# Optimization experiments

Hardware: AMD Instinct MI355X
Metric: run time of the kernel (lower is better)

Reference implementation:

```python
import jax, jax.numpy as jnp
import numpy as np

DECAY = 0.99
EPSILON = 1e-05
CODEBOOK_SIZE = 1024


def setup_inputs() -> dict:
    key = jax.random.key(0)
    k1, k2, k3 = jax.random.split(key, 3)
    B, T, D, K = 8, 4096, 128, CODEBOOK_SIZE
    return {
        "x": jax.random.normal(k1, (B, T, D), dtype=jnp.float32),
        "embed": jax.random.normal(k2, (K, D), dtype=jnp.float32),
        "cluster_size": jnp.ones((K,), dtype=jnp.float32),
        "embed_avg": jax.random.normal(k3, (K, D), dtype=jnp.float32),
    }


def reference(x, embed, cluster_size, embed_avg):
    shape = x.shape
    K, D = embed.shape
    flat = x.reshape(-1, D)  # (N, D)

    dist = 2.0 * (flat @ embed.T) - jnp.sum(flat * flat, axis=1, keepdims=True) \
           - jnp.sum(embed * embed, axis=1)[None, :]  # (N, K)
    embed_ind_flat = jnp.argmax(dist, axis=-1)  # (N,) int
    embed_ind = embed_ind_flat.reshape(shape[:-1])
    quantize = embed[embed_ind]  # dequantize via gather, (B, T, D)

    # training EMA updates (one-hot scatter expressed as segment sums)
    counts = jax.ops.segment_sum(jnp.ones_like(embed_ind_flat, dtype=x.dtype),
                                 embed_ind_flat, num_segments=K)  # == onehot.sum(0)
    embed_sum = jax.ops.segment_sum(flat, embed_ind_flat, num_segments=K)  # == (x.T @ onehot).T

    new_cluster_size = cluster_size * DECAY + (1.0 - DECAY) * counts
    new_embed_avg = embed_avg * DECAY + (1.0 - DECAY) * embed_sum

    total = new_cluster_size.sum()
    smoothed = (new_cluster_size + EPSILON) / (total + K * EPSILON) * total
    new_embed = new_embed_avg / smoothed[:, None]

    return quantize, embed_ind, new_cluster_size, new_embed_avg, new_embed
```

## Files before the change

### kernel.cpp

```cpp
#include <hip/hip_runtime.h>

#define NROWS 32768
#define DDIM  128
#define KCODES 1024
#define DECAY 0.99f
#define OMD   0.01f
#define EPS   1e-5f

typedef __attribute__((ext_vector_type(8))) short short8;
typedef __attribute__((ext_vector_type(4))) float f32x4;

#define WS_COUNTS 0
#define WS_OFFS   1024
#define WS_CURSOR 2048
#define WS_INV    3072
#define WS_EN2H   4096
#define WS_BUCKET 5120

__device__ __forceinline__ unsigned short f2bf(float f) {
  union { float f; unsigned int u; } cv; cv.f = f;
  unsigned int u = cv.u;
  return (unsigned short)((u + 0x7fffu + ((u >> 16) & 1u)) >> 16);
}

__global__ __launch_bounds__(256) void pack_e(const float* __restrict__ embed,
                                              ushort* __restrict__ epack,
                                              float* __restrict__ en2h) {
  const int tid = threadIdx.x;
  const int w = tid >> 6, lane = tid & 63;
  const int nt = blockIdx.x * 4 + w;
  const int m = lane & 15, q = lane >> 4;
  const int row = nt * 16 + m;
  const float* ep = embed + (size_t)row * DDIM + q * 8;
  float ss = 0.f;
  #pragma unroll
  for (int kb = 0; kb < 4; ++kb) {
    float4 v0 = *(const float4*)(ep + kb * 32);
    float4 v1 = *(const float4*)(ep + kb * 32 + 4);
    float v[8] = {v0.x, v0.y, v0.z, v0.w, v1.x, v1.y, v1.z, v1.w};
    unsigned int h[8], l[8];
    #pragma unroll
    for (int j = 0; j < 8; ++j) {
      ss += v[j] * v[j];
      h[j] = f2bf(v[j]);
      float fh = __uint_as_float(h[j] << 16);
      l[j] = f2bf(v[j] - fh);
    }
    uint4 ph, pl;
    ph.x = h[0] | (h[1] << 16); ph.y = h[2] | (h[3] << 16);
    ph.z = h[4] | (h[5] << 16); ph.w = h[6] | (h[7] << 16);
    pl.x = l[0] | (l[1] << 16); pl.y = l[2] | (l[3] << 16);
    pl.z = l[4] | (l[5] << 16); pl.w = l[6] | (l[7] << 16);
    *(uint4*)(epack + (((size_t)nt * 8 + kb) * 64 + lane) * 8)     = ph;
    *(uint4*)(epack + (((size_t)nt * 8 + kb + 4) * 64 + lane) * 8) = pl;
  }
  ss += __shfl_xor(ss, 16, 64);
  ss += __shfl_xor(ss, 32, 64);
  if (q == 0) en2h[row] = 0.5f * ss;
}

__global__ __launch_bounds__(256)
__attribute__((amdgpu_waves_per_eu(2, 2)))
void vq_mfma(
    const float* __restrict__ x, const short8* __restrict__ ep8,
    const float* __restrict__ en2h,
    float* __restrict__ counts, float* __restrict__ out_ind) {
  __shared__ unsigned long long keys[4][64];
  const int tid = threadIdx.x;
  const int w = tid >> 6, lane = tid & 63;
  const int c = lane & 15, q = lane >> 4;
  const int mt0 = blockIdx.x * 4;
  const int nt0 = w * 16;

  short8 a[4][8];
  #pragma unroll
  for (int t = 0; t < 4; ++t) {
    const float* xp = x + (size_t)((mt0 + t) * 16 + c) * DDIM + q * 8;
    #pragma unroll
    for (int kb = 0; kb < 4; ++kb) {
      float4 v0 = *(const float4*)(xp + kb * 32);
      float4 v1 = *(const float4*)(xp + kb * 32 + 4);
      float v[8] = {v0.x, v0.y, v0.z, v0.w, v1.x, v1.y, v1.z, v1.w};
      short8 hh, ll;
      #pragma unroll
      for (int j = 0; j < 8; ++j) {
        unsigned int hv = f2bf(v[j]);
        hh[j] = (short)hv;
        float fh = __uint_as_float(hv << 16);
        ll[j] = (short)f2bf(v[j] - fh);
      }
      a[t][kb] = hh;
      a[t][kb + 4] = ll;
    }
  }

  float bestv[16]; int besti[16];
  #pragma unroll
  for (int i = 0; i < 16; ++i) { bestv[i] = -3.4e38f; besti[i] = 0; }

  for (int ch = 0; ch < 16; ++ch) {
    const int nt = nt0 + ch;
    short8 st[8];
    #pragma unroll
    for (int j = 0; j < 8; ++j)
      st[j] = ep8[((size_t)nt * 8 + j) * 64 + lane];
    const float nh = en2h[nt * 16 + c];
    f32x4 acc[4];
    #pragma unroll
    for (int t = 0; t < 4; ++t) acc[t] = (f32x4){0.f, 0.f, 0.f, 0.f};
    #pragma unroll
    for (int t = 0; t < 4; ++t) {
      #pragma unroll
      for (int kb = 0; kb < 4; ++kb)
        acc[t] = __builtin_amdgcn_mfma_f32_16x16x32_bf16(a[t][kb], st[kb], acc[t], 0, 0, 0);
      #pragma unroll
      for (int kb = 0; kb < 4; ++kb)
        acc[t] = __builtin_amdgcn_mfma_f32_16x16x32_bf16(a[t][4 + kb], st[kb], acc[t], 0, 0, 0);
      #pragma unroll
      for (int kb = 0; kb < 4; ++kb)
        acc[t] = __builtin_amdgcn_mfma_f32_16x16x32_bf16(a[t][kb], st[4 + kb], acc[t], 0, 0, 0);
    }
    const int code = nt * 16 + c;
    #pragma unroll
    for (int t = 0; t < 4; ++t)
      #pragma unroll
      for (int r = 0; r < 4; ++r) {
        float s = acc[t][r] - nh;
        int i = t * 4 + r;
        if (s > bestv[i]) { bestv[i] = s; besti[i] = code; }
      }
  }

  #pragma unroll
  for (int off = 1; off < 16; off <<= 1) {
    #pragma unroll
    for (int i = 0; i < 16; ++i) {
      float ov = __shfl_xor(bestv[i], off, 64);
      int   oi = __shfl_xor(besti[i], off, 64);
      if (ov > bestv[i] || (ov == bestv[i] && oi < besti[i])) {
        bestv[i] = ov; besti[i] = oi;
      }
    }
  }
  if (c == 0) {
    #pragma unroll
    for (int t = 0; t < 4; ++t)
      #pragma unroll
      for (int r = 0; r < 4; ++r) {
        unsigned u = __float_as_uint(bestv[t * 4 + r]);
        unsigned su = (u & 0x80000000u) ? ~u : (u | 0x80000000u);
        keys[w][t * 16 + q * 4 + r] =
            ((unsigned long long)su << 32) |
            (unsigned long long)(0xFFFFFFFFu - (unsigned)besti[t * 4 + r]);
      }
  }
  __syncthreads();
  if (tid < 64) {
    unsigned long long k0 = keys[0][tid], k1 = keys[1][tid];
    unsigned long long k2 = keys[2][tid], k3 = keys[3][tid];
    unsigned long long k = k0 > k1 ? k0 : k1;
    if (k2 > k) k = k2;
    if (k3 > k) k = k3;
    int code = (int)(0xFFFFFFFFu - (unsigned)(k & 0xFFFFFFFFull));
    out_ind[blockIdx.x * 64 + tid] = (float)code;
    unsafeAtomicAdd(counts + code, 1.0f);
  }
}

__global__ void scan_fin(const float* __restrict__ counts, const float* __restrict__ cs,
                         int* __restrict__ offs, int* __restrict__ cursor,
                         float* __restrict__ out_ncs, float* __restrict__ inv) {
  __shared__ float wtot[16];
  __shared__ float ctot[16];
  int tid = threadIdx.x;
  int lane = tid & 63, w = tid >> 6;
  float cnum = counts[tid];
  float cv = cs[tid];
  float s = cnum;
  #pragma unroll
  for (int off = 1; off < 64; off <<= 1) {
    float v = __shfl_up(s, off, 64);
    if (lane >= off) s += v;
  }
  float r2 = cv;
  #pragma unroll
  for (int off = 32; off > 0; off >>= 1) r2 += __shfl_down(r2, off, 64);
  if (lane == 63) wtot[w] = s;
  if (lane == 0)  ctot[w] = r2;
  __syncthreads();
  if (tid < 16) {
    float v = wtot[tid];
    #pragma unroll
    for (int off = 1; off < 16; off <<= 1) {
      float p = __shfl_up(v, off, 64);
      if (tid >= off) v += p;
    }
    wtot[tid] = v;
    float t2 = ctot[tid];
    #pragma unroll
    for (int off = 8; off > 0; off >>= 1) t2 += __shfl_down(t2, off, 64);
    if (tid == 0) ctot[0] = t2;
  }
  __syncthreads();
  float prefix = (w > 0) ? wtot[w - 1] : 0.f;
  int excl = (int)(s + prefix) - (int)cnum;
  offs[tid] = excl;
  cursor[tid] = excl;
  float ncs = cv * DECAY + OMD * cnum;
  out_ncs[tid] = ncs;
  float total = ctot[0] * DECAY + OMD * (float)NROWS;
  inv[tid] = (total + (float)KCODES * EPS) / ((ncs + EPS) * total);
}

__global__ void scatter_rows(const float* __restrict__ out_ind,
                             int* __restrict__ cursor, int* __restrict__ bucket) {
  int row = blockIdx.x * 256 + threadIdx.x;
  int code = (int)out_ind[row];
  int pos = atomicAdd(cursor + code, 1);
  bucket[pos] = row;
}

__global__ __launch_bounds__(256) void esum_q_fin(
    const int* __restrict__ bucket, const int* __restrict__ offs,
    const float* __restrict__ counts, const float* __restrict__ x,
    const float* __restrict__ embed, const float* __restrict__ ea,
    const float* __restrict__ inv,
    float* __restrict__ out_q, float* __restrict__ out_nea, float* __restrict__ out_ne) {
  __shared__ float4 part[512];
  const int code = blockIdx.x;
  const int t = threadIdx.x;
  const int c8 = t & 15;
  const int h = t >> 4;
  const int start = offs[code];
  const int cnt = (int)counts[code];
  const float4 e0 = *(const float4*)(embed + (size_t)code * DDIM + c8 * 8);
  const float4 e1 = *(const float4*)(embed + (size_t)code * DDIM + c8 * 8 + 4);
  float4 a0 = {0.f, 0.f, 0.f, 0.f}, a1 = {0.f, 0.f, 0.f, 0.f};
  int i = h;
  for (; i + 16 < cnt; i += 32) {
    int rowA = bucket[start + i];
    int rowB = bucket[start + i + 16];
    const float* pa = x + (size_t)rowA * DDIM + c8 * 8;
    const float* pb = x + (size_t)rowB * DDIM + c8 * 8;
    float4 xa0 = *(const float4*)(pa), xa1 = *(const float4*)(pa + 4);
    float4 xb0 = *(const float4*)(pb), xb1 = *(const float4*)(pb + 4);
    float* qa = out_q + (size_t)rowA * DDIM + c8 * 8;
    float* qb = out_q + (size_t)rowB * DDIM + c8 * 8;
    *(float4*)(qa) = e0; *(float4*)(qa + 4) = e1;
    *(float4*)(qb) = e0; *(float4*)(qb + 4) = e1;
    a0.x += xa0.x + xb0.x; a0.y += xa0.y + xb0.y; a0.z += xa0.z + xb0.z; a0.w += xa0.w + xb0.w;
    a1.x += xa1.x + xb1.x; a1.y += xa1.y + xb1.y; a1.z += xa1.z + xb1.z; a1.w += xa1.w + xb1.w;
  }
  for (; i < cnt; i += 16) {
    int row = bucket[start + i];
    const float* pa = x + (size_t)row * DDIM + c8 * 8;
    float4 xa0 = *(const float4*)(pa), xa1 = *(const float4*)(pa + 4);
    float* qa = out_q + (size_t)row * DDIM + c8 * 8;
    *(float4*)(qa) = e0; *(float4*)(qa + 4) = e1;
    a0.x += xa0.x; a0.y += xa0.y; a0.z += xa0.z; a0.w += xa0.w;
    a1.x += xa1.x; a1.y += xa1.y; a1.z += xa1.z; a1.w += xa1.w;
  }
  part[h * 32 + c8 * 2]     = a0;
  part[h * 32 + c8 * 2 + 1] = a1;
  __syncthreads();
  if (t < 32) {
    float4 s = part[t];
    #pragma unroll
    for (int hh = 1; hh < 16; ++hh) {
      float4 p = part[hh * 32 + t];
      s.x += p.x; s.y += p.y; s.z += p.z; s.w += p.w;
    }
    float iv = inv[code];
    int base = code * DDIM + t * 4;
    float4 a = *(const float4*)(ea + base);
    float4 nea;
    nea.x = a.x * DECAY + OMD * s.x; nea.y = a.y * DECAY + OMD * s.y;
    nea.z = a.z * DECAY + OMD * s.z; nea.w = a.w * DECAY + OMD * s.w;
    *(float4*)(out_nea + base) = nea;
    float4 ne;
    ne.x = nea.x * iv; ne.y = nea.y * iv; ne.z = nea.z * iv; ne.w = nea.w * iv;
    *(float4*)(out_ne + base) = ne;
  }
}

extern "C" void kernel_launch(void* const* d_in, const int* in_sizes, int n_in,
                              void* d_out, int out_size, void* d_ws, size_t ws_size,
                              hipStream_t stream) {
  const float* x     = (const float*)d_in[0];
  const float* embed = (const float*)d_in[1];
  const float* cs    = (const float*)d_in[2];
  const float* ea    = (const float*)d_in[3];

  float* out     = (float*)d_out;
  float* out_q   = out;
  float* out_ind = out_q + 4194304;
  float* out_ncs = out_ind + 32768;
  float* out_nea = out_ncs + 1024;
  float* out_ne  = out_nea + 131072;

  float* ws     = (float*)d_ws;
  float* counts = ws + WS_COUNTS;
  int*   offs   = (int*)(ws + WS_OFFS);
  int*   cursor = (int*)(ws + WS_CURSOR);
  float* inv    = ws + WS_INV;
  float* en2h   = ws + WS_EN2H;
  int*   bucket = (int*)(ws + WS_BUCKET);

  ushort* epack = (ushort*)out_nea;

  hipMemsetAsync(counts, 0, KCODES * sizeof(float), stream);
  pack_e<<<16, 256, 0, stream>>>(embed, epack, en2h);
  vq_mfma<<<NROWS / 64, 256, 0, stream>>>(x, (const short8*)epack, en2h, counts, out_ind);
  scan_fin<<<1, 1024, 0, stream>>>(counts, cs, offs, cursor, out_ncs, inv);
  scatter_rows<<<NROWS / 256, 256, 0, stream>>>(out_ind, cursor, bucket);
  esum_q_fin<<<KCODES, 256, 0, stream>>>(bucket, offs, counts, x, embed, ea, inv,
                                         out_q, out_nea, out_ne);
}
```

Baseline: 184.8 us.

## Fuse codebook packing into VQ kernel and merge histogram, scan and scatter

Removes the separate pack_e kernel: each wave now loads fp32 codebook rows directly, computes their half-norms and splits them into bf16 hi/lo inside the distance loop. M-tile per block drops from 64 to 32 rows, which doubles the grid and reduces accumulator registers. The global-atomic count, scan and scatter kernels become one single-block kernel that builds the histogram and bucket list with shared-memory atomics. This removes a memset and three launches, but the codebook is now re-converted by every block, and the bucket scatter runs serially in a single workgroup.

```diff
diff --git a/kernel.cpp b/kernel.cpp
--- a/kernel.cpp
+++ b/kernel.cpp
@@ -12,69 +12,27 @@
 
 #define WS_COUNTS 0
 #define WS_OFFS   1024
-#define WS_CURSOR 2048
-#define WS_INV    3072
-#define WS_EN2H   4096
-#define WS_BUCKET 5120
-
-__device__ __forceinline__ unsigned short f2bf(float f) {
+#define WS_INV    2048
+#define WS_BUCKET 3072
+
+__device__ __forceinline__ unsigned int f2bf(float f) {
   union { float f; unsigned int u; } cv; cv.f = f;
   unsigned int u = cv.u;
-  return (unsigned short)((u + 0x7fffu + ((u >> 16) & 1u)) >> 16);
-}
-
-__global__ __launch_bounds__(256) void pack_e(const float* __restrict__ embed,
-                                              ushort* __restrict__ epack,
-                                              float* __restrict__ en2h) {
-  const int tid = threadIdx.x;
-  const int w = tid >> 6, lane = tid & 63;
-  const int nt = blockIdx.x * 4 + w;
-  const int m = lane & 15, q = lane >> 4;
-  const int row = nt * 16 + m;
-  const float* ep = embed + (size_t)row * DDIM + q * 8;
-  float ss = 0.f;
-  #pragma unroll
-  for (int kb = 0; kb < 4; ++kb) {
-    float4 v0 = *(const float4*)(ep + kb * 32);
-    float4 v1 = *(const float4*)(ep + kb * 32 + 4);
-    float v[8] = {v0.x, v0.y, v0.z, v0.w, v1.x, v1.y, v1.z, v1.w};
-    unsigned int h[8], l[8];
-    #pragma unroll
-    for (int j = 0; j < 8; ++j) {
-      ss += v[j] * v[j];
-      h[j] = f2bf(v[j]);
-      float fh = __uint_as_float(h[j] << 16);
-      l[j] = f2bf(v[j] - fh);
-    }
-    uint4 ph, pl;
-    ph.x = h[0] | (h[1] << 16); ph.y = h[2] | (h[3] << 16);
-    ph.z = h[4] | (h[5] << 16); ph.w = h[6] | (h[7] << 16);
-    pl.x = l[0] | (l[1] << 16); pl.y = l[2] | (l[3] << 16);
-    pl.z = l[4] | (l[5] << 16); pl.w = l[6] | (l[7] << 16);
-    *(uint4*)(epack + (((size_t)nt * 8 + kb) * 64 + lane) * 8)     = ph;
-    *(uint4*)(epack + (((size_t)nt * 8 + kb + 4) * 64 + lane) * 8) = pl;
-  }
-  ss += __shfl_xor(ss, 16, 64);
-  ss += __shfl_xor(ss, 32, 64);
-  if (q == 0) en2h[row] = 0.5f * ss;
-}
-
-__global__ __launch_bounds__(256)
-__attribute__((amdgpu_waves_per_eu(2, 2)))
-void vq_mfma(
-    const float* __restrict__ x, const short8* __restrict__ ep8,
-    const float* __restrict__ en2h,
-    float* __restrict__ counts, float* __restrict__ out_ind) {
-  __shared__ unsigned long long keys[4][64];
+  return (u + 0x7fffu + ((u >> 16) & 1u)) >> 16;
+}
+
+__global__ __launch_bounds__(256) void vq_mfma(
+    const float* __restrict__ x, const float* __restrict__ embed,
+    float* __restrict__ out_ind) {
+  __shared__ unsigned long long keys[4][32];
   const int tid = threadIdx.x;
   const int w = tid >> 6, lane = tid & 63;
   const int c = lane & 15, q = lane >> 4;
-  const int mt0 = blockIdx.x * 4;
-  const int nt0 = w * 16;
-
-  short8 a[4][8];
-  #pragma unroll
-  for (int t = 0; t < 4; ++t) {
+  const int mt0 = blockIdx.x * 2;
+
+  short8 a[2][8];
+  #pragma unroll
+  for (int t = 0; t < 2; ++t) {
     const float* xp = x + (size_t)((mt0 + t) * 16 + c) * DDIM + q * 8;
     #pragma unroll
     for (int kb = 0; kb < 4; ++kb) {
@@ -94,47 +52,66 @@
     }
   }
 
-  float bestv[16]; int besti[16];
-  #pragma unroll
-  for (int i = 0; i < 16; ++i) { bestv[i] = -3.4e38f; besti[i] = 0; }
-
+  float bestv[8]; int besti[8];
+  #pragma unroll
+  for (int i = 0; i < 8; ++i) { bestv[i] = -3.4e38f; besti[i] = 0; }
+
+  const int cbase = w * 256;
   for (int ch = 0; ch < 16; ++ch) {
-    const int nt = nt0 + ch;
-    short8 st[8];
-    #pragma unroll
-    for (int j = 0; j < 8; ++j)
-      st[j] = ep8[((size_t)nt * 8 + j) * 64 + lane];
-    const float nh = en2h[nt * 16 + c];
-    f32x4 acc[4];
-    #pragma unroll
-    for (int t = 0; t < 4; ++t) acc[t] = (f32x4){0.f, 0.f, 0.f, 0.f};
-    #pragma unroll
-    for (int t = 0; t < 4; ++t) {
+    const int crow = cbase + ch * 16 + c;
+    const float* ep = embed + (size_t)crow * DDIM + q * 8;
+    float nhq = 0.f;
+    short8 sh[4], sl[4];
+    #pragma unroll
+    for (int kb = 0; kb < 4; ++kb) {
+      float4 v0 = *(const float4*)(ep + kb * 32);
+      float4 v1 = *(const float4*)(ep + kb * 32 + 4);
+      float v[8] = {v0.x, v0.y, v0.z, v0.w, v1.x, v1.y, v1.z, v1.w};
+      short8 hh, ll;
       #pragma unroll
-      for (int kb = 0; kb < 4; ++kb)
-        acc[t] = __builtin_amdgcn_mfma_f32_16x16x32_bf16(a[t][kb], st[kb], acc[t], 0, 0, 0);
-      #pragma unroll
-      for (int kb = 0; kb < 4; ++kb)
-        acc[t] = __builtin_amdgcn_mfma_f32_16x16x32_bf16(a[t][4 + kb], st[kb], acc[t], 0, 0, 0);
-      #pragma unroll
-      for (int kb = 0; kb < 4; ++kb)
-        acc[t] = __builtin_amdgcn_mfma_f32_16x16x32_bf16(a[t][kb], st[4 + kb], acc[t], 0, 0, 0);
-    }
-    const int code = nt * 16 + c;
-    #pragma unroll
-    for (int t = 0; t < 4; ++t)
-      #pragma unroll
-      for (int r = 0; r < 4; ++r) {
-        float s = acc[t][r] - nh;
-        int i = t * 4 + r;
-        if (s > bestv[i]) { bestv[i] = s; besti[i] = code; }
-      }
+      for (int j = 0; j < 8; ++j) {
+        nhq += v[j] * v[j];
+        unsigned int hv = f2bf(v[j]);
+        hh[j] = (short)hv;
+        float fh = __uint_as_float(hv << 16);
+        ll[j] = (short)f2bf(v[j] - fh);
+      }
+      sh[kb] = hh;
+      sl[kb] = ll;
+    }
+    nhq += __shfl_xor(nhq, 16, 64);
+    nhq += __shfl_xor(nhq, 32, 64);
+    const float nh = 0.5f * nhq;
+
+    f32x4 acc0 = {0.f, 0.f, 0.f, 0.f}, acc1 = {0.f, 0.f, 0.f, 0.f};
+    #pragma unroll
+    for (int kb = 0; kb < 4; ++kb) {
+      acc0 = __builtin_amdgcn_mfma_f32_16x16x32_bf16(a[0][kb], sh[kb], acc0, 0, 0, 0);
+      acc1 = __builtin_amdgcn_mfma_f32_16x16x32_bf16(a[1][kb], sh[kb], acc1, 0, 0, 0);
+    }
+    #pragma unroll
+    for (int kb = 0; kb < 4; ++kb) {
+      acc0 = __builtin_amdgcn_mfma_f32_16x16x32_bf16(a[0][kb + 4], sh[kb], acc0, 0, 0, 0);
+      acc1 = __builtin_amdgcn_mfma_f32_16x16x32_bf16(a[1][kb + 4], sh[kb], acc1, 0, 0, 0);
+    }
+    #pragma unroll
+    for (int kb = 0; kb < 4; ++kb) {
+      acc0 = __builtin_amdgcn_mfma_f32_16x16x32_bf16(a[0][kb], sl[kb], acc0, 0, 0, 0);
+      acc1 = __builtin_amdgcn_mfma_f32_16x16x32_bf16(a[1][kb], sl[kb], acc1, 0, 0, 0);
+    }
+    #pragma unroll
+    for (int r = 0; r < 4; ++r) {
+      float s0 = acc0[r] - nh;
+      if (s0 > bestv[r])     { bestv[r] = s0;     besti[r] = crow; }
+      float s1 = acc1[r] - nh;
+      if (s1 > bestv[4 + r]) { bestv[4 + r] = s1; besti[4 + r] = crow; }
+    }
   }
 
   #pragma unroll
   for (int off = 1; off < 16; off <<= 1) {
     #pragma unroll
-    for (int i = 0; i < 16; ++i) {
+    for (int i = 0; i < 8; ++i) {
       float ov = __shfl_xor(bestv[i], off, 64);
       int   oi = __shfl_xor(besti[i], off, 64);
       if (ov > bestv[i] || (ov == bestv[i] && oi < besti[i])) {
@@ -144,7 +121,7 @@
   }
   if (c == 0) {
     #pragma unroll
-    for (int t = 0; t < 4; ++t)
+    for (int t = 0; t < 2; ++t)
       #pragma unroll
       for (int r = 0; r < 4; ++r) {
         unsigned u = __float_as_uint(bestv[t * 4 + r]);
@@ -155,27 +132,38 @@
       }
   }
   __syncthreads();
-  if (tid < 64) {
+  if (tid < 32) {
     unsigned long long k0 = keys[0][tid], k1 = keys[1][tid];
     unsigned long long k2 = keys[2][tid], k3 = keys[3][tid];
     unsigned long long k = k0 > k1 ? k0 : k1;
     if (k2 > k) k = k2;
     if (k3 > k) k = k3;
     int code = (int)(0xFFFFFFFFu - (unsigned)(k & 0xFFFFFFFFull));
-    out_ind[blockIdx.x * 64 + tid] = (float)code;
-    unsafeAtomicAdd(counts + code, 1.0f);
-  }
-}
-
-__global__ void scan_fin(const float* __restrict__ counts, const float* __restrict__ cs,
-                         int* __restrict__ offs, int* __restrict__ cursor,
-                         float* __restrict__ out_ncs, float* __restrict__ inv) {
-  __shared__ float wtot[16];
-  __shared__ float ctot[16];
-  int tid = threadIdx.x;
-  int lane = tid & 63, w = tid >> 6;
-  float cnum = counts[tid];
-  float cv = cs[tid];
+    out_ind[blockIdx.x * 32 + tid] = (float)code;
+  }
+}
+
+__global__ __launch_bounds__(1024) void scanall(
+    const float* __restrict__ out_ind, const float* __restrict__ cs,
+    float* __restrict__ counts_g, int* __restrict__ offs, float* __restrict__ inv,
+    int* __restrict__ bucket, float* __restrict__ out_ncs) {
+  __shared__ int hist[1024];
+  __shared__ int cur[1024];
+  __shared__ float wtot[16], ctot[16];
+  const int tid = threadIdx.x;
+  const int lane = tid & 63, w = tid >> 6;
+  int codes[32];
+  hist[tid] = 0;
+  __syncthreads();
+  #pragma unroll
+  for (int i = 0; i < 32; ++i) {
+    codes[i] = (int)out_ind[i * 1024 + tid];
+    atomicAdd(&hist[codes[i]], 1);
+  }
+  __syncthreads();
+  const int cnt = hist[tid];
+  const float cnum = (float)cnt;
+  const float cv = cs[tid];
   float s = cnum;
   #pragma unroll
   for (int off = 1; off < 64; off <<= 1) {
@@ -202,22 +190,21 @@
     if (tid == 0) ctot[0] = t2;
   }
   __syncthreads();
-  float prefix = (w > 0) ? wtot[w - 1] : 0.f;
-  int excl = (int)(s + prefix) - (int)cnum;
+  const float prefix = (w > 0) ? wtot[w - 1] : 0.f;
+  const int excl = (int)(s + prefix) - cnt;
   offs[tid] = excl;
-  cursor[tid] = excl;
-  float ncs = cv * DECAY + OMD * cnum;
+  cur[tid] = excl;
+  counts_g[tid] = cnum;
+  const float ncs = cv * DECAY + OMD * cnum;
   out_ncs[tid] = ncs;
-  float total = ctot[0] * DECAY + OMD * (float)NROWS;
+  const float total = ctot[0] * DECAY + OMD * (float)NROWS;
   inv[tid] = (total + (float)KCODES * EPS) / ((ncs + EPS) * total);
-}
-
-__global__ void scatter_rows(const float* __restrict__ out_ind,
-                             int* __restrict__ cursor, int* __restrict__ bucket) {
-  int row = blockIdx.x * 256 + threadIdx.x;
-  int code = (int)out_ind[row];
-  int pos = atomicAdd(cursor + code, 1);
-  bucket[pos] = row;
+  __syncthreads();
+  #pragma unroll
+  for (int i = 0; i < 32; ++i) {
+    int pos = atomicAdd(&cur[codes[i]], 1);
+    bucket[pos] = i * 1024 + tid;
+  }
 }
 
 __global__ __launch_bounds__(256) void esum_q_fin(
@@ -301,18 +288,11 @@
   float* ws     = (float*)d_ws;
   float* counts = ws + WS_COUNTS;
   int*   offs   = (int*)(ws + WS_OFFS);
-  int*   cursor = (int*)(ws + WS_CURSOR);
   float* inv    = ws + WS_INV;
-  float* en2h   = ws + WS_EN2H;
   int*   bucket = (int*)(ws + WS_BUCKET);
 
-  ushort* epack = (ushort*)out_nea;
-
-  hipMemsetAsync(counts, 0, KCODES * sizeof(float), stream);
-  pack_e<<<16, 256, 0, stream>>>(embed, epack, en2h);
-  vq_mfma<<<NROWS / 64, 256, 0, stream>>>(x, (const short8*)epack, en2h, counts, out_ind);
-  scan_fin<<<1, 1024, 0, stream>>>(counts, cs, offs, cursor, out_ncs, inv);
-  scatter_rows<<<NROWS / 256, 256, 0, stream>>>(out_ind, cursor, bucket);
+  vq_mfma<<<NROWS / 32, 256, 0, stream>>>(x, embed, out_ind);
+  scanall<<<1, 1024, 0, stream>>>(out_ind, cs, counts, offs, inv, bucket, out_ncs);
   esum_q_fin<<<KCODES, 256, 0, stream>>>(bucket, offs, counts, x, embed, ea, inv,
                                          out_q, out_nea, out_ne);
 }
```

Result: slower. 202.0 us (+9.3%).

## Fuse quantize gather into VQ kernel, histogram counts in scan, halve rows per block

Applied to the files above, without the earlier changes.

The VQ MFMA kernel now handles 32 rows per block instead of 64, which doubles the grid and drops the forced waves-per-EU limit. It also writes the gathered quantized rows straight from embed. Per-code counts come from an LDS histogram built in the single-block scan kernel, which removes the global atomics and the memset. The segment-sum kernel no longer scatters out_q. In exchange, codebook tiles are reloaded per block with less reuse, and the single-block histogram serializes 32K reads onto one CU.

```diff
diff --git a/kernel.cpp b/kernel.cpp
--- a/kernel.cpp
+++ b/kernel.cpp
@@ -17,10 +17,10 @@
 #define WS_EN2H   4096
 #define WS_BUCKET 5120
 
-__device__ __forceinline__ unsigned short f2bf(float f) {
+__device__ __forceinline__ unsigned int f2bf(float f) {
   union { float f; unsigned int u; } cv; cv.f = f;
   unsigned int u = cv.u;
-  return (unsigned short)((u + 0x7fffu + ((u >> 16) & 1u)) >> 16);
+  return (u + 0x7fffu + ((u >> 16) & 1u)) >> 16;
 }
 
 __global__ __launch_bounds__(256) void pack_e(const float* __restrict__ embed,
@@ -59,22 +59,20 @@
   if (q == 0) en2h[row] = 0.5f * ss;
 }
 
-__global__ __launch_bounds__(256)
-__attribute__((amdgpu_waves_per_eu(2, 2)))
-void vq_mfma(
+__global__ __launch_bounds__(256) void vq_mfma(
     const float* __restrict__ x, const short8* __restrict__ ep8,
-    const float* __restrict__ en2h,
-    float* __restrict__ counts, float* __restrict__ out_ind) {
-  __shared__ unsigned long long keys[4][64];
+    const float* __restrict__ en2h, const float* __restrict__ embed,
+    float* __restrict__ out_ind, float* __restrict__ out_q) {
+  __shared__ unsigned long long keys[4][32];
+  __shared__ int scodes[32];
   const int tid = threadIdx.x;
   const int w = tid >> 6, lane = tid & 63;
   const int c = lane & 15, q = lane >> 4;
-  const int mt0 = blockIdx.x * 4;
-  const int nt0 = w * 16;
-
-  short8 a[4][8];
-  #pragma unroll
-  for (int t = 0; t < 4; ++t) {
+  const int mt0 = blockIdx.x * 2;
+
+  short8 a[2][8];
+  #pragma unroll
+  for (int t = 0; t < 2; ++t) {
     const float* xp = x + (size_t)((mt0 + t) * 16 + c) * DDIM + q * 8;
     #pragma unroll
     for (int kb = 0; kb < 4; ++kb) {
@@ -94,10 +92,11 @@
     }
   }
 
-  float bestv[16]; int besti[16];
-  #pragma unroll
-  for (int i = 0; i < 16; ++i) { bestv[i] = -3.4e38f; besti[i] = 0; }
-
+  float bestv[8]; int besti[8];
+  #pragma unroll
+  for (int i = 0; i < 8; ++i) { bestv[i] = -3.4e38f; besti[i] = 0; }
+
+  const int nt0 = w * 16;
   for (int ch = 0; ch < 16; ++ch) {
     const int nt = nt0 + ch;
     short8 st[8];
@@ -105,36 +104,36 @@
     for (int j = 0; j < 8; ++j)
       st[j] = ep8[((size_t)nt * 8 + j) * 64 + lane];
     const float nh = en2h[nt * 16 + c];
-    f32x4 acc[4];
-    #pragma unroll
-    for (int t = 0; t < 4; ++t) acc[t] = (f32x4){0.f, 0.f, 0.f, 0.f};
-    #pragma unroll
-    for (int t = 0; t < 4; ++t) {
-      #pragma unroll
-      for (int kb = 0; kb < 4; ++kb)
-        acc[t] = __builtin_amdgcn_mfma_f32_16x16x32_bf16(a[t][kb], st[kb], acc[t], 0, 0, 0);
-      #pragma unroll
-      for (int kb = 0; kb < 4; ++kb)
-        acc[t] = __builtin_amdgcn_mfma_f32_16x16x32_bf16(a[t][4 + kb], st[kb], acc[t], 0, 0, 0);
-      #pragma unroll
-      for (int kb = 0; kb < 4; ++kb)
-        acc[t] = __builtin_amdgcn_mfma_f32_16x16x32_bf16(a[t][kb], st[4 + kb], acc[t], 0, 0, 0);
+    f32x4 acc0 = {0.f, 0.f, 0.f, 0.f}, acc1 = {0.f, 0.f, 0.f, 0.f};
+    #pragma unroll
+    for (int kb = 0; kb < 4; ++kb) {
+      acc0 = __builtin_amdgcn_mfma_f32_16x16x32_bf16(a[0][kb], st[kb], acc0, 0, 0, 0);
+      acc1 = __builtin_amdgcn_mfma_f32_16x16x32_bf16(a[1][kb], st[kb], acc1, 0, 0, 0);
+    }
+    #pragma unroll
+    for (int kb = 0; kb < 4; ++kb) {
+      acc0 = __builtin_amdgcn_mfma_f32_16x16x32_bf16(a[0][kb + 4], st[kb], acc0, 0, 0, 0);
+      acc1 = __builtin_amdgcn_mfma_f32_16x16x32_bf16(a[1][kb + 4], st[kb], acc1, 0, 0, 0);
+    }
+    #pragma unroll
+    for (int kb = 0; kb < 4; ++kb) {
+      acc0 = __builtin_amdgcn_mfma_f32_16x16x32_bf16(a[0][kb], st[kb + 4], acc0, 0, 0, 0);
+      acc1 = __builtin_amdgcn_mfma_f32_16x16x32_bf16(a[1][kb], st[kb + 4], acc1, 0, 0, 0);
     }
     const int code = nt * 16 + c;
     #pragma unroll
-    for (int t = 0; t < 4; ++t)
-      #pragma unroll
-      for (int r = 0; r < 4; ++r) {
-        float s = acc[t][r] - nh;
-        int i = t * 4 + r;
-        if (s > bestv[i]) { bestv[i] = s; besti[i] = code; }
-      }
+    for (int r = 0; r < 4; ++r) {
+      float s0 = acc0[r] - nh;
+      if (s0 > bestv[r])     { bestv[r] = s0;     besti[r] = code; }
+      float s1 = acc1[r] - nh;
+      if (s1 > bestv[4 + r]) { bestv[4 + r] = s1; besti[4 + r] = code; }
+    }
   }
 
   #pragma unroll
   for (int off = 1; off < 16; off <<= 1) {
     #pragma unroll
-    for (int i = 0; i < 16; ++i) {
+    for (int i = 0; i < 8; ++i) {
       float ov = __shfl_xor(bestv[i], off, 64);
       int   oi = __shfl_xor(besti[i], off, 64);
       if (ov > bestv[i] || (ov == bestv[i] && oi < besti[i])) {
@@ -144,7 +143,7 @@
   }
   if (c == 0) {
     #pragma unroll
-    for (int t = 0; t < 4; ++t)
+    for (int t = 0; t < 2; ++t)
       #pragma unroll
       for (int r = 0; r < 4; ++r) {
         unsigned u = __float_as_uint(bestv[t * 4 + r]);
@@ -155,27 +154,44 @@
       }
   }
   __syncthreads();
-  if (tid < 64) {
+  if (tid < 32) {
     unsigned long long k0 = keys[0][tid], k1 = keys[1][tid];
     unsigned long long k2 = keys[2][tid], k3 = keys[3][tid];
     unsigned long long k = k0 > k1 ? k0 : k1;
     if (k2 > k) k = k2;
     if (k3 > k) k = k3;
     int code = (int)(0xFFFFFFFFu - (unsigned)(k & 0xFFFFFFFFull));
-    out_ind[blockIdx.x * 64 + tid] = (float)code;
-    unsafeAtomicAdd(counts + code, 1.0f);
-  }
-}
-
-__global__ void scan_fin(const float* __restrict__ counts, const float* __restrict__ cs,
-                         int* __restrict__ offs, int* __restrict__ cursor,
-                         float* __restrict__ out_ncs, float* __restrict__ inv) {
-  __shared__ float wtot[16];
-  __shared__ float ctot[16];
-  int tid = threadIdx.x;
-  int lane = tid & 63, w = tid >> 6;
-  float cnum = counts[tid];
-  float cv = cs[tid];
+    out_ind[blockIdx.x * 32 + tid] = (float)code;
+    scodes[tid] = code;
+  }
+  __syncthreads();
+  #pragma unroll
+  for (int it = 0; it < 4; ++it) {
+    int idx = tid + it * 256;
+    int row = idx >> 5, c4 = idx & 31;
+    int code = scodes[row];
+    *(float4*)(out_q + (size_t)(blockIdx.x * 32 + row) * DDIM + c4 * 4) =
+        *(const float4*)(embed + (size_t)code * DDIM + c4 * 4);
+  }
+}
+
+__global__ __launch_bounds__(1024) void scan_fin(
+    const float* __restrict__ out_ind, const float* __restrict__ cs,
+    float* __restrict__ counts_g, int* __restrict__ offs, int* __restrict__ cursor,
+    float* __restrict__ inv, float* __restrict__ out_ncs) {
+  __shared__ int hist[1024];
+  __shared__ float wtot[16], ctot[16];
+  const int tid = threadIdx.x;
+  const int lane = tid & 63, w = tid >> 6;
+  hist[tid] = 0;
+  __syncthreads();
+  #pragma unroll
+  for (int i = 0; i < 32; ++i)
+    atomicAdd(&hist[(int)out_ind[i * 1024 + tid]], 1);
+  __syncthreads();
+  const int cnt = hist[tid];
+  const float cnum = (float)cnt;
+  const float cv = cs[tid];
   float s = cnum;
   #pragma unroll
   for (int off = 1; off < 64; off <<= 1) {
@@ -202,13 +218,14 @@
     if (tid == 0) ctot[0] = t2;
   }
   __syncthreads();
-  float prefix = (w > 0) ? wtot[w - 1] : 0.f;
-  int excl = (int)(s + prefix) - (int)cnum;
+  const float prefix = (w > 0) ? wtot[w - 1] : 0.f;
+  const int excl = (int)(s + prefix) - cnt;
   offs[tid] = excl;
   cursor[tid] = excl;
-  float ncs = cv * DECAY + OMD * cnum;
+  counts_g[tid] = cnum;
+  const float ncs = cv * DECAY + OMD * cnum;
   out_ncs[tid] = ncs;
-  float total = ctot[0] * DECAY + OMD * (float)NROWS;
+  const float total = ctot[0] * DECAY + OMD * (float)NROWS;
   inv[tid] = (total + (float)KCODES * EPS) / ((ncs + EPS) * total);
 }
 
@@ -220,12 +237,11 @@
   bucket[pos] = row;
 }
 
-__global__ __launch_bounds__(256) void esum_q_fin(
+__global__ __launch_bounds__(256) void esum_fin(
     const int* __restrict__ bucket, const int* __restrict__ offs,
     const float* __restrict__ counts, const float* __restrict__ x,
-    const float* __restrict__ embed, const float* __restrict__ ea,
-    const float* __restrict__ inv,
-    float* __restrict__ out_q, float* __restrict__ out_nea, float* __restrict__ out_ne) {
+    const float* __restrict__ ea, const float* __restrict__ inv,
+    float* __restrict__ out_nea, float* __restrict__ out_ne) {
   __shared__ float4 part[512];
   const int code = blockIdx.x;
   const int t = threadIdx.x;
@@ -233,8 +249,6 @@
   const int h = t >> 4;
   const int start = offs[code];
   const int cnt = (int)counts[code];
-  const float4 e0 = *(const float4*)(embed + (size_t)code * DDIM + c8 * 8);
-  const float4 e1 = *(const float4*)(embed + (size_t)code * DDIM + c8 * 8 + 4);
   float4 a0 = {0.f, 0.f, 0.f, 0.f}, a1 = {0.f, 0.f, 0.f, 0.f};
   int i = h;
   for (; i + 16 < cnt; i += 32) {
@@ -244,10 +258,6 @@
     const float* pb = x + (size_t)rowB * DDIM + c8 * 8;
     float4 xa0 = *(const float4*)(pa), xa1 = *(const float4*)(pa + 4);
     float4 xb0 = *(const float4*)(pb), xb1 = *(const float4*)(pb + 4);
-    float* qa = out_q + (size_t)rowA * DDIM + c8 * 8;
-    float* qb = out_q + (size_t)rowB * DDIM + c8 * 8;
-    *(float4*)(qa) = e0; *(float4*)(qa + 4) = e1;
-    *(float4*)(qb) = e0; *(float4*)(qb + 4) = e1;
     a0.x += xa0.x + xb0.x; a0.y += xa0.y + xb0.y; a0.z += xa0.z + xb0.z; a0.w += xa0.w + xb0.w;
     a1.x += xa1.x + xb1.x; a1.y += xa1.y + xb1.y; a1.z += xa1.z + xb1.z; a1.w += xa1.w + xb1.w;
   }
@@ -255,8 +265,6 @@
     int row = bucket[start + i];
     const float* pa = x + (size_t)row * DDIM + c8 * 8;
     float4 xa0 = *(const float4*)(pa), xa1 = *(const float4*)(pa + 4);
-    float* qa = out_q + (size_t)row * DDIM + c8 * 8;
-    *(float4*)(qa) = e0; *(float4*)(qa + 4) = e1;
     a0.x += xa0.x; a0.y += xa0.y; a0.z += xa0.z; a0.w += xa0.w;
     a1.x += xa1.x; a1.y += xa1.y; a1.z += xa1.z; a1.w += xa1.w;
   }
@@ -308,11 +316,11 @@
 
   ushort* epack = (ushort*)out_nea;
 
-  hipMemsetAsync(counts, 0, KCODES * sizeof(float), stream);
   pack_e<<<16, 256, 0, stream>>>(embed, epack, en2h);
-  vq_mfma<<<NROWS / 64, 256, 0, stream>>>(x, (const short8*)epack, en2h, counts, out_ind);
-  scan_fin<<<1, 1024, 0, stream>>>(counts, cs, offs, cursor, out_ncs, inv);
+  vq_mfma<<<NROWS / 32, 256, 0, stream>>>(x, (const short8*)epack, en2h, embed,
+                                          out_ind, out_q);
+  scan_fin<<<1, 1024, 0, stream>>>(out_ind, cs, counts, offs, cursor, inv, out_ncs);
   scatter_rows<<<NROWS / 256, 256, 0, stream>>>(out_ind, cursor, bucket);
-  esum_q_fin<<<KCODES, 256, 0, stream>>>(bucket, offs, counts, x, embed, ea, inv,
-                                         out_q, out_nea, out_ne);
-}
+  esum_fin<<<KCODES, 256, 0, stream>>>(bucket, offs, counts, x, ea, inv,
+                                       out_nea, out_ne);
+}
```

Measured after the change: 171.3 us. 7.3% less time.
